# Kernel tuning notes

Measured on AMD Instinct MI355X. Metric: run time of the kernel, lower is better.

The kernel has to match this reference:

```python
import jax, jax.numpy as jnp
import numpy as np

B, N, ADA, L, D_OUT, C_T, N_DIS = 8, 2048, 16, 64, 16, 4, 8
H = L // D_OUT  # 4 heads emulated via split/cat on the batch dim


def setup_inputs() -> dict:
    key = jax.random.key(0)
    ks = jax.random.split(key, 12)
    f = lambda i, shape, s=1.0: jax.random.normal(ks[i], shape, dtype=jnp.float32) * s
    return dict(
        c=f(0, (B, N, L)),
        c_condition=f(1, (B, C_T)),
        c_disease=f(2, (B, N_DIS)),
        state=f(3, (B, N, L)),
        emb_normal=f(4, (N, ADA)),                 # nn.Parameter embeddings_normal
        W_q1=f(5, (C_T, L), 0.1), b_q1=jnp.zeros((L,), jnp.float32),
        W_qr1=f(6, (1, L), 0.1),  b_qr1=jnp.zeros((L,), jnp.float32),
        W_q2=f(7, (L, L), 0.1),   b_q2=jnp.zeros((L,), jnp.float32),
        W_qr2=f(8, (L, L), 0.1),  b_qr2=jnp.zeros((L,), jnp.float32),
        Wp_gcn=f(9, (ADA, 2, L, L), 0.1),          # adaptive weight pool (cheb_k=2)
        bp_gcn=f(10, (ADA, L), 0.1),               # adaptive bias pool
    )


def _to_heads(t):
    # torch.cat(torch.split(t, D_OUT, dim=-1), dim=0): [B,N,H*d] -> [H*B,N,d]
    return jnp.concatenate(jnp.split(t, H, axis=-1), axis=0)


def _from_heads(t):
    # inverse: [H*B,N,d] -> [B,N,H*d]
    return jnp.concatenate(jnp.split(t, H, axis=0), axis=-1)


def _anode_gcn(x, E, Wp, bp):
    # adaptive GCN (AGCRN-style AVWGCN): supports=[I, softmax(relu(E E^T))]
    A = jax.nn.softmax(jax.nn.relu(E @ E.T), axis=1)          # [N,N]
    xg = jnp.stack([x, jnp.einsum('nm,bmc->bnc', A, x)], 1)   # [B,2,N,C]
    Wn = jnp.einsum('nd,dkio->nkio', E, Wp)                   # per-node weights
    bn = E @ bp                                               # [N,L]
    return jnp.einsum('bkni,nkio->bno', xg, Wn) + bn


def reference(c, c_condition, c_disease, state, emb_normal,
              W_q1, b_q1, W_qr1, b_qr1, W_q2, b_q2, W_qr2, b_qr2,
              Wp_gcn, bp_gcn):
    # gated query path
    Qt = jax.nn.sigmoid(c_condition[:, None, :] @ W_q1 + b_q1)        # [B,1,L]
    Qt = jnp.tanh((Qt * c) @ W_q2 + b_q2)                             # [B,N,L]
    # disease loop vectorized: sum_n sigmoid(Linear(c_disease[:, n:n+1]))
    qr = jax.nn.sigmoid(c_disease[:, :, None] * W_qr1[0] + b_qr1)     # [B,D,L]
    qr = qr.sum(axis=1, keepdims=True)                                # [B,1,L]
    qr = Qt + jnp.tanh((qr * c) @ W_qr2 + b_qr2)                      # [B,N,L]
    qr_h = _to_heads(qr)  # computed in the original but unused in output

    theta = _to_heads(state)                                          # [HB,N,d]
    ct = jnp.tanh(_anode_gcn(c, emb_normal, Wp_gcn, bp_gcn))          # [B,N,L]
    ct = _to_heads(ct)                                                # [HB,N,d]

    attn = jnp.einsum('bnd,bmd->bnm', theta, theta) / jnp.sqrt(jnp.float32(D_OUT))
    attn = jax.nn.softmax(attn, axis=-1)                              # [HB,N,N]
    x = -jnp.einsum('bnm,bmd->bnd', attn, ct)                         # [HB,N,d]
    return _from_heads(x)                                             # [B,N,L]
```

## Files before the change

### kernel.cpp

```cpp
#include <hip/hip_runtime.h>
#include <hip/hip_bf16.h>

#define NN 2048
#define BB 8
#define LL 64
#define ADA 16
#define DH 16
#define HB 32
#define KT 2048
#define CGSZ ((size_t)BB * NN * LL)

typedef __attribute__((ext_vector_type(4))) short bf16x4;
typedef __attribute__((ext_vector_type(4))) float f32x4;
typedef _Float16 half_t;
typedef __attribute__((ext_vector_type(2))) _Float16 halfx2;
typedef __attribute__((ext_vector_type(4))) _Float16 halfx4;
typedef __attribute__((ext_vector_type(8))) _Float16 halfx8;

#if defined(__HIP_DEVICE_COMPILE__)
#if __has_builtin(__builtin_amdgcn_mfma_f32_16x16x16f16)
#define MFMA16H(a, b, c) __builtin_amdgcn_mfma_f32_16x16x16f16(a, b, c, 0, 0, 0)
#elif __has_builtin(__builtin_amdgcn_mfma_f32_16x16x16_f16)
#define MFMA16H(a, b, c) __builtin_amdgcn_mfma_f32_16x16x16_f16(a, b, c, 0, 0, 0)
#else
#error "no 16x16x16 f16 mfma builtin on device"
#endif
#if __has_builtin(__builtin_amdgcn_mfma_f32_16x16x32_f16)
#define MFMA32H(a, b, c) __builtin_amdgcn_mfma_f32_16x16x32_f16(a, b, c, 0, 0, 0)
#else
#error "no 16x16x32 f16 mfma builtin on device"
#endif
#if __has_builtin(__builtin_amdgcn_exp2f)
#define EXP2F(x) __builtin_amdgcn_exp2f(x)
#else
#define EXP2F(x) exp2f(x)
#endif
#else
#define MFMA16H(a, b, c) (c)
#define MFMA32H(a, b, c) (c)
#define EXP2F(x) exp2f(x)
#endif

__device__ inline halfx2 cvt_pk2(float a, float b) {
#if defined(__HIP_DEVICE_COMPILE__) && __has_builtin(__builtin_amdgcn_cvt_pkrtz)
  auto r = __builtin_amdgcn_cvt_pkrtz(a, b);
  return __builtin_bit_cast(halfx2, r);
#else
  halfx2 r;
  r[0] = (_Float16)a;
  r[1] = (_Float16)b;
  return r;
#endif
}

__device__ inline float tanh_fast(float v) {
  return 1.f - 2.f / (__expf(2.f * v) + 1.f);
}

__global__ __launch_bounds__(256) void k_preps(const float* __restrict__ E,
                                               const float* __restrict__ c,
                                               const float* __restrict__ state,
                                               const float* __restrict__ Wp,
                                               half_t* __restrict__ A16,
                                               half_t* __restrict__ cT16,
                                               half_t* __restrict__ WpT,
                                               half_t* __restrict__ th16h,
                                               half_t* __restrict__ thq16h) {
  __shared__ float sbuf[4 * 2304];
  const int id = blockIdx.x;
  const int t = threadIdx.x;
  if (id < 512) {
    float(*row)[NN] = (float(*)[NN])sbuf;
    float(*red)[256] = (float(*)[256])(sbuf + 4 * NN);
    const int n = id * 4;
    float4 e[4][4];
#pragma unroll
    for (int r = 0; r < 4; ++r) {
      const float4* Er = (const float4*)(E + (size_t)(n + r) * ADA);
#pragma unroll
      for (int j = 0; j < 4; ++j) e[r][j] = Er[j];
    }
    float l[4] = {0.f, 0.f, 0.f, 0.f};
    for (int m = t; m < NN; m += 256) {
      const float4* Em = (const float4*)(E + (size_t)m * ADA);
      float4 ev[4];
#pragma unroll
      for (int j = 0; j < 4; ++j) ev[j] = Em[j];
#pragma unroll
      for (int r = 0; r < 4; ++r) {
        float s = 0.f;
#pragma unroll
        for (int j = 0; j < 4; ++j) {
          s = fmaf(e[r][j].x, ev[j].x, s);
          s = fmaf(e[r][j].y, ev[j].y, s);
          s = fmaf(e[r][j].z, ev[j].z, s);
          s = fmaf(e[r][j].w, ev[j].w, s);
        }
        float p = __expf(fmaxf(s, 0.f) - 20.f);
        row[r][m] = p;
        l[r] += p;
      }
    }
#pragma unroll
    for (int r = 0; r < 4; ++r) red[r][t] = l[r];
    __syncthreads();
    for (int off = 128; off > 0; off >>= 1) {
      if (t < off) {
#pragma unroll
        for (int r = 0; r < 4; ++r) red[r][t] += red[r][t + off];
      }
      __syncthreads();
    }
    float inv[4];
#pragma unroll
    for (int r = 0; r < 4; ++r) inv[r] = 1.f / red[r][0];
    for (int m = t; m < NN; m += 256) {
#pragma unroll
      for (int r = 0; r < 4; ++r)
        A16[(size_t)(n + r) * NN + m] = (half_t)(row[r][m] * inv[r]);
    }
  } else if (id < 768) {
    float(*ld)[68] = (float(*)[68])sbuf;
    const int idx = id - 512;
    const int m0 = (idx & 31) * 64;
    const int b = idx >> 5;
    {
      const int r = t & 63, cq = t >> 6;
      const float* cp = c + ((size_t)b * NN + m0 + r) * LL + cq * 16;
#pragma unroll
      for (int u = 0; u < 4; ++u)
        *(float4*)&ld[r][cq * 16 + 4 * u] = *(const float4*)(cp + 4 * u);
    }
    __syncthreads();
    const int o = t & 63, mq = t >> 6;
    halfx8 h0, h1;
#pragma unroll
    for (int v = 0; v < 8; ++v) {
      h0[v] = (half_t)ld[mq * 16 + v][o];
      h1[v] = (half_t)ld[mq * 16 + 8 + v][o];
    }
    half_t* op = cT16 + ((size_t)b * LL + o) * NN + m0 + mq * 16;
    *(halfx8*)op = h0;
    *(halfx8*)(op + 8) = h1;
  } else if (id < 800) {
    float(*ld)[68] = (float(*)[68])sbuf;
    const int k0 = (id - 768) * 64;
    {
      const int r = t & 63, cq = t >> 6;
      const float* wp = Wp + (size_t)(k0 + r) * LL + cq * 16;
#pragma unroll
      for (int u = 0; u < 4; ++u)
        *(float4*)&ld[r][cq * 16 + 4 * u] = *(const float4*)(wp + 4 * u);
    }
    __syncthreads();
    const int o = t & 63, kq = t >> 6;
    halfx8 h0, h1;
#pragma unroll
    for (int v = 0; v < 8; ++v) {
      h0[v] = (half_t)ld[kq * 16 + v][o];
      h1[v] = (half_t)ld[kq * 16 + 8 + v][o];
    }
    half_t* op = WpT + (size_t)o * KT + k0 + kq * 16;
    *(halfx8*)op = h0;
    *(halfx8*)(op + 8) = h1;
  } else {
    const int idx = id - 800;
    const int n0 = (idx & 31) * 64;
    const int b = idx >> 5;
    const int r = t >> 2, h = t & 3;
    const float QS = 0.25f * 1.4426950408889634f;
    const float* sp = state + ((size_t)b * NN + n0 + r) * LL + h * DH;
    half_t tk[16], tq[16];
#pragma unroll
    for (int u = 0; u < 4; ++u) {
      float4 sv = *(const float4*)(sp + 4 * u);
      tk[4 * u + 0] = (half_t)sv.x; tk[4 * u + 1] = (half_t)sv.y;
      tk[4 * u + 2] = (half_t)sv.z; tk[4 * u + 3] = (half_t)sv.w;
      tq[4 * u + 0] = (half_t)(QS * sv.x); tq[4 * u + 1] = (half_t)(QS * sv.y);
      tq[4 * u + 2] = (half_t)(QS * sv.z); tq[4 * u + 3] = (half_t)(QS * sv.w);
    }
    const size_t base = ((size_t)(h * 8 + b) * NN + n0 + r) * DH;
    *(halfx8*)(th16h + base) = *(const halfx8*)&tk[0];
    *(halfx8*)(th16h + base + 8) = *(const halfx8*)&tk[8];
    *(halfx8*)(thq16h + base) = *(const halfx8*)&tq[0];
    *(halfx8*)(thq16h + base + 8) = *(const halfx8*)&tq[8];
  }
}

__global__ __launch_bounds__(256) void k_gemm1b(const half_t* __restrict__ A16,
                                                const half_t* __restrict__ cT16,
                                                float* __restrict__ cg) {
  __shared__ half_t sA[64][72];
  __shared__ half_t sB[2][64][72];
  const int t = threadIdx.x;
  const int n0 = blockIdx.x * 64;
  const int b0 = blockIdx.y * 2;
  const int kh = blockIdx.z;
  const int wv = t >> 6, lane = t & 63;
  const int lr = lane & 15, lg = lane >> 4;
  const half_t* cb0 = cT16 + (size_t)b0 * LL * NN;
  const half_t* cb1 = cb0 + (size_t)LL * NN;
  const int sr = t >> 2, sc = (t & 3) * 16;
  f32x4 acc[2][4];
#pragma unroll
  for (int bb = 0; bb < 2; ++bb)
#pragma unroll
    for (int ot = 0; ot < 4; ++ot) acc[bb][ot] = (f32x4){0.f, 0.f, 0.f, 0.f};

  for (int k0 = kh * (NN / 4); k0 < (kh + 1) * (NN / 4); k0 += 64) {
    __syncthreads();
    {
      const half_t* ga = A16 + (size_t)(n0 + sr) * NN + k0 + sc;
      *(halfx8*)&sA[sr][sc] = *(const halfx8*)ga;
      *(halfx8*)&sA[sr][sc + 8] = *(const halfx8*)(ga + 8);
      const half_t* g0 = cb0 + (size_t)sr * NN + k0 + sc;
      *(halfx8*)&sB[0][sr][sc] = *(const halfx8*)g0;
      *(halfx8*)&sB[0][sr][sc + 8] = *(const halfx8*)(g0 + 8);
      const half_t* g1 = cb1 + (size_t)sr * NN + k0 + sc;
      *(halfx8*)&sB[1][sr][sc] = *(const halfx8*)g1;
      *(halfx8*)&sB[1][sr][sc + 8] = *(const halfx8*)(g1 + 8);
    }
    __syncthreads();
#pragma unroll
    for (int kt = 0; kt < 2; ++kt) {
      halfx8 a = *(const halfx8*)&sA[16 * wv + lr][kt * 32 + 8 * lg];
#pragma unroll
      for (int bb = 0; bb < 2; ++bb) {
#pragma unroll
        for (int ot = 0; ot < 4; ++ot) {
          halfx8 bq = *(const halfx8*)&sB[bb][ot * 16 + lr][kt * 32 + 8 * lg];
          acc[bb][ot] = MFMA32H(a, bq, acc[bb][ot]);
        }
      }
    }
  }
#pragma unroll
  for (int bb = 0; bb < 2; ++bb) {
    float* outp = cg + (size_t)kh * CGSZ + ((size_t)(b0 + bb) * NN + n0 + 16 * wv) * LL;
#pragma unroll
    for (int ot = 0; ot < 4; ++ot)
#pragma unroll
      for (int reg = 0; reg < 4; ++reg)
        outp[(size_t)(4 * lg + reg) * LL + ot * 16 + lr] = acc[bb][ot][reg];
  }
}

__global__ __launch_bounds__(256) void k_gcn4(const float* __restrict__ E,
                                              const half_t* __restrict__ WpT,
                                              const float* __restrict__ bp,
                                              const float* __restrict__ c,
                                              const float* __restrict__ cg,
                                              half_t* __restrict__ vt16h) {
  __shared__ half_t sW[32][136];
  __shared__ float sE[64][17];
  __shared__ float sbp[16][32];
  const int t = threadIdx.x;
  const int n0 = blockIdx.x * 64;
  const int b = blockIdx.y;
  const int oh = blockIdx.z;
  const int wv = t >> 6, lane = t & 63;
  const int lr = lane & 15, lg = lane >> 4;
  {
    const int r = t >> 2, dq = (t & 3) * 4;
    float4 ev = *(const float4*)(E + (size_t)(n0 + r) * ADA + dq);
    sE[r][dq + 0] = ev.x; sE[r][dq + 1] = ev.y;
    sE[r][dq + 2] = ev.z; sE[r][dq + 3] = ev.w;
    const int d = t >> 4, o2 = (t & 15) * 2;
    float2 bv = *(const float2*)(bp + d * LL + oh * 32 + o2);
    sbp[d][o2] = bv.x;
    sbp[d][o2 + 1] = bv.y;
  }
  float xr[4][8];
  {
    const size_t rbase = ((size_t)b * NN + n0 + 16 * wv + lr) * LL;
#pragma unroll
    for (int u = 0; u < 2; ++u) {
      const float* p = c + rbase + u * 32 + 8 * lg;
      float4 v0 = *(const float4*)p, v1 = *(const float4*)(p + 4);
      xr[u][0] = v0.x; xr[u][1] = v0.y; xr[u][2] = v0.z; xr[u][3] = v0.w;
      xr[u][4] = v1.x; xr[u][5] = v1.y; xr[u][6] = v1.z; xr[u][7] = v1.w;
    }
#pragma unroll
    for (int u = 0; u < 2; ++u) {
      const size_t off = rbase + u * 32 + 8 * lg;
      float4 a0 = *(const float4*)(cg + off), a1 = *(const float4*)(cg + off + 4);
      float4 b0 = *(const float4*)(cg + CGSZ + off), b1 = *(const float4*)(cg + CGSZ + off + 4);
      float4 c0 = *(const float4*)(cg + 2 * CGSZ + off), c1 = *(const float4*)(cg + 2 * CGSZ + off + 4);
      float4 d0 = *(const float4*)(cg + 3 * CGSZ + off), d1 = *(const float4*)(cg + 3 * CGSZ + off + 4);
      xr[2 + u][0] = (a0.x + b0.x) + (c0.x + d0.x);
      xr[2 + u][1] = (a0.y + b0.y) + (c0.y + d0.y);
      xr[2 + u][2] = (a0.z + b0.z) + (c0.z + d0.z);
      xr[2 + u][3] = (a0.w + b0.w) + (c0.w + d0.w);
      xr[2 + u][4] = (a1.x + b1.x) + (c1.x + d1.x);
      xr[2 + u][5] = (a1.y + b1.y) + (c1.y + d1.y);
      xr[2 + u][6] = (a1.z + b1.z) + (c1.z + d1.z);
      xr[2 + u][7] = (a1.w + b1.w) + (c1.w + d1.w);
    }
  }
  __syncthreads();
  f32x4 acc[2];
#pragma unroll
  for (int ot2 = 0; ot2 < 2; ++ot2) {
    f32x4 s = (f32x4){0.f, 0.f, 0.f, 0.f};
#pragma unroll
    for (int d = 0; d < ADA; ++d) {
      const float bpv = sbp[d][ot2 * 16 + lr];
#pragma unroll
      for (int reg = 0; reg < 4; ++reg)
        s[reg] = fmaf(sE[16 * wv + 4 * lg + reg][d], bpv, s[reg]);
    }
    acc[ot2] = s;
  }
  const int so = t >> 3, sq = t & 7;
  halfx8 wreg[2];
  {
    const half_t* p = WpT + (size_t)(oh * 32 + so) * KT + sq * 16;
    wreg[0] = *(const halfx8*)p;
    wreg[1] = *(const halfx8*)(p + 8);
  }
  for (int dd = 0; dd < ADA; ++dd) {
    __syncthreads();
    *(halfx8*)&sW[so][sq * 16] = wreg[0];
    *(halfx8*)&sW[so][sq * 16 + 8] = wreg[1];
    __syncthreads();
    if (dd < ADA - 1) {
      const half_t* p = WpT + (size_t)(oh * 32 + so) * KT + (dd + 1) * 128 + sq * 16;
      wreg[0] = *(const halfx8*)p;
      wreg[1] = *(const halfx8*)(p + 8);
    }
    const float e = sE[16 * wv + lr][dd];
    halfx8 af[4];
#pragma unroll
    for (int kt = 0; kt < 4; ++kt)
#pragma unroll
      for (int j = 0; j < 8; ++j) af[kt][j] = (half_t)(e * xr[kt][j]);
#pragma unroll
    for (int kt = 0; kt < 4; ++kt) {
#pragma unroll
      for (int ot2 = 0; ot2 < 2; ++ot2) {
        halfx8 bq = *(const halfx8*)&sW[ot2 * 16 + lr][kt * 32 + 8 * lg];
        acc[ot2] = MFMA32H(af[kt], bq, acc[ot2]);
      }
    }
  }
#pragma unroll
  for (int ot2 = 0; ot2 < 2; ++ot2) {
    const int h = oh * 2 + ot2;
    halfx4 o4;
#pragma unroll
    for (int reg = 0; reg < 4; ++reg) o4[reg] = (half_t)tanh_fast(acc[ot2][reg]);
    *(halfx4*)(vt16h + ((size_t)(h * 8 + b) * DH + lr) * NN + n0 + 16 * wv + 4 * lg) = o4;
  }
}

__global__ __launch_bounds__(512, 4) void k_attn5(const half_t* __restrict__ th16h,
                                                  const half_t* __restrict__ thq16h,
                                                  const half_t* __restrict__ vt16h,
                                                  float* __restrict__ out) {
  __shared__ float sred[8][8][16][16];
  float* dfl = &sred[0][0][0][0];
  const int hb = blockIdx.x;
  const int h = hb >> 3, b = hb & 7;
  const int wv = threadIdx.x >> 6, lane = threadIdx.x & 63;
  const int q0 = blockIdx.y * 128;
  const int lr = lane & 15, lg = lane >> 4;
  const half_t* th = th16h + (size_t)hb * NN * DH;
  const half_t* thq = thq16h + (size_t)hb * NN * DH;
  const half_t* vrow = vt16h + ((size_t)hb * DH + lr) * NN;
  halfx4 qf[8];
#pragma unroll
  for (int f = 0; f < 8; ++f)
    qf[f] = *(const halfx4*)(thq + (size_t)(q0 + 16 * f + lr) * DH + 4 * lg);
  const float SH = 8.f * 1.4426950408889634f;
  const f32x4 shiftv = {-SH, -SH, -SH, -SH};
  f32x4 acc[8];
  float den[8];
#pragma unroll
  for (int f = 0; f < 8; ++f) { acc[f] = (f32x4){0.f, 0.f, 0.f, 0.f}; den[f] = 0.f; }

  const int mb = wv * (NN / 8);
  halfx4 kf = *(const halfx4*)(th + (size_t)(mb + lr) * DH + 4 * lg);
  halfx4 vf = *(const halfx4*)(vrow + mb + 4 * lg);
  for (int mt = 0; mt < NN / 128; ++mt) {
    halfx4 kf_n = kf, vf_n = vf;
    if (mt < NN / 128 - 1) {
      const int mn = mb + (mt + 1) * 16;
      kf_n = *(const halfx4*)(th + (size_t)(mn + lr) * DH + 4 * lg);
      vf_n = *(const halfx4*)(vrow + mn + 4 * lg);
    }
#pragma unroll
    for (int f = 0; f < 8; ++f) {
      f32x4 s = MFMA16H(kf, qf[f], shiftv);
      float p0 = EXP2F(s[0]), p1 = EXP2F(s[1]), p2 = EXP2F(s[2]), p3 = EXP2F(s[3]);
      den[f] += (p0 + p1) + (p2 + p3);
      halfx2 lo = cvt_pk2(p0, p1), hi = cvt_pk2(p2, p3);
      halfx4 pf;
      pf[0] = lo[0]; pf[1] = lo[1]; pf[2] = hi[0]; pf[3] = hi[1];
      acc[f] = MFMA16H(pf, vf, acc[f]);
    }
    kf = kf_n; vf = vf_n;
  }
#pragma unroll
  for (int f = 0; f < 8; ++f) {
    den[f] += __shfl_xor(den[f], 16);
    den[f] += __shfl_xor(den[f], 32);
  }
  if (lane < 16) {
#pragma unroll
    for (int f = 0; f < 8; ++f) dfl[(wv * 8 + f) * 16 + lane] = den[f];
  }
  __syncthreads();
  const int t = threadIdx.x;
  const int fo = t >> 6, ro = (t >> 2) & 15, duo = (t & 3) * 4;
  float ds = 0.f;
#pragma unroll
  for (int w = 0; w < 8; ++w) ds += dfl[(w * 8 + fo) * 16 + ro];
  __syncthreads();
#pragma unroll
  for (int f = 0; f < 8; ++f) {
#pragma unroll
    for (int reg = 0; reg < 4; ++reg) sred[wv][f][4 * lg + reg][lr] = acc[f][reg];
  }
  __syncthreads();
  float4 ns = make_float4(0.f, 0.f, 0.f, 0.f);
#pragma unroll
  for (int w = 0; w < 8; ++w) {
    float4 v = *(const float4*)&sred[w][fo][ro][duo];
    ns.x += v.x; ns.y += v.y; ns.z += v.z; ns.w += v.w;
  }
  const float inv = -1.f / ds;
  float4 o = make_float4(ns.x * inv, ns.y * inv, ns.z * inv, ns.w * inv);
  *(float4*)(out + ((size_t)b * NN + q0 + 16 * fo + ro) * LL + h * DH + duo) = o;
}

extern "C" void kernel_launch(void* const* d_in, const int* in_sizes, int n_in,
                              void* d_out, int out_size, void* d_ws, size_t ws_size,
                              hipStream_t stream) {
  const float* c = (const float*)d_in[0];
  const float* state = (const float*)d_in[3];
  const float* E = (const float*)d_in[4];
  const float* Wp = (const float*)d_in[13];
  const float* bp = (const float*)d_in[14];
  float* out = (float*)d_out;

  half_t* A16 = (half_t*)d_ws;
  half_t* cT16 = A16 + (size_t)NN * NN;
  half_t* WpT = cT16 + (size_t)BB * LL * NN;
  float* cg = (float*)(WpT + (size_t)LL * KT);
  half_t* th16h = (half_t*)(cg + 4 * CGSZ);
  half_t* thq16h = th16h + (size_t)HB * NN * DH;
  half_t* vt16h = thq16h + (size_t)HB * NN * DH;

  k_preps<<<1056, 256, 0, stream>>>(E, c, state, Wp, A16, cT16, WpT, th16h, thq16h);
  k_gemm1b<<<dim3(NN / 64, BB / 2, 4), 256, 0, stream>>>(A16, cT16, cg);
  k_gcn4<<<dim3(NN / 64, BB, 2), 256, 0, stream>>>(E, WpT, bp, c, cg, vt16h);
  k_attn5<<<dim3(HB, NN / 128), 512, 0, stream>>>(th16h, thq16h, vt16h, out);
}
```

Before: 67.87 us.

## Split attention key range across two blocks with separate reduction kernel

The attention kernel now splits the key dimension into two halves via a third grid dimension. Each block writes partial numerators and denominators to workspace, and a new reduction kernel combines them, normalizes, and writes the output. This doubles the block count from 512 to 1024 so the GPU is better occupied. The cost is an extra launch plus partial-sum traffic through global memory. The fixed exp shift keeps the split-softmax combination exact.

```diff
diff --git a/kernel.cpp b/kernel.cpp
--- a/kernel.cpp
+++ b/kernel.cpp
@@ -353,16 +353,17 @@
   }
 }
 
-__global__ __launch_bounds__(512, 4) void k_attn5(const half_t* __restrict__ th16h,
+__global__ __launch_bounds__(512, 4) void k_attn6(const half_t* __restrict__ th16h,
                                                   const half_t* __restrict__ thq16h,
                                                   const half_t* __restrict__ vt16h,
-                                                  float* __restrict__ out) {
+                                                  float* __restrict__ npart,
+                                                  float* __restrict__ dpart) {
   __shared__ float sred[8][8][16][16];
   float* dfl = &sred[0][0][0][0];
   const int hb = blockIdx.x;
-  const int h = hb >> 3, b = hb & 7;
   const int wv = threadIdx.x >> 6, lane = threadIdx.x & 63;
   const int q0 = blockIdx.y * 128;
+  const int mz = blockIdx.z;
   const int lr = lane & 15, lg = lane >> 4;
   const half_t* th = th16h + (size_t)hb * NN * DH;
   const half_t* thq = thq16h + (size_t)hb * NN * DH;
@@ -378,12 +379,12 @@
 #pragma unroll
   for (int f = 0; f < 8; ++f) { acc[f] = (f32x4){0.f, 0.f, 0.f, 0.f}; den[f] = 0.f; }
 
-  const int mb = wv * (NN / 8);
+  const int mb = mz * (NN / 2) + wv * (NN / 16);
   halfx4 kf = *(const halfx4*)(th + (size_t)(mb + lr) * DH + 4 * lg);
   halfx4 vf = *(const halfx4*)(vrow + mb + 4 * lg);
-  for (int mt = 0; mt < NN / 128; ++mt) {
+  for (int mt = 0; mt < NN / 256; ++mt) {
     halfx4 kf_n = kf, vf_n = vf;
-    if (mt < NN / 128 - 1) {
+    if (mt < NN / 256 - 1) {
       const int mn = mb + (mt + 1) * 16;
       kf_n = *(const halfx4*)(th + (size_t)(mn + lr) * DH + 4 * lg);
       vf_n = *(const halfx4*)(vrow + mn + 4 * lg);
@@ -428,9 +429,28 @@
     float4 v = *(const float4*)&sred[w][fo][ro][duo];
     ns.x += v.x; ns.y += v.y; ns.z += v.z; ns.w += v.w;
   }
+  const int q = q0 + 16 * fo + ro;
+  *(float4*)(npart + (((size_t)mz * HB + hb) * NN + q) * DH + duo) = ns;
+  if (duo == 0) dpart[((size_t)mz * HB + hb) * NN + q] = ds;
+}
+
+__global__ __launch_bounds__(256) void k_red(const float* __restrict__ npart,
+                                             const float* __restrict__ dpart,
+                                             float* __restrict__ out) {
+  const int idx = blockIdx.x * 256 + threadIdx.x;
+  const int row = idx >> 2;
+  const int du = (idx & 3) * 4;
+  const int hb = row >> 11, q = row & 2047;
+  const int h = hb >> 3, b = hb & 7;
+  const size_t base0 = ((size_t)row) * DH + du;
+  const size_t base1 = ((size_t)HB * NN + row) * DH + du;
+  float4 n0 = *(const float4*)(npart + base0);
+  float4 n1 = *(const float4*)(npart + base1);
+  const float ds = dpart[row] + dpart[(size_t)HB * NN + row];
   const float inv = -1.f / ds;
-  float4 o = make_float4(ns.x * inv, ns.y * inv, ns.z * inv, ns.w * inv);
-  *(float4*)(out + ((size_t)b * NN + q0 + 16 * fo + ro) * LL + h * DH + duo) = o;
+  float4 o = make_float4((n0.x + n1.x) * inv, (n0.y + n1.y) * inv,
+                         (n0.z + n1.z) * inv, (n0.w + n1.w) * inv);
+  *(float4*)(out + ((size_t)b * NN + q) * LL + h * DH + du) = o;
 }
 
 extern "C" void kernel_launch(void* const* d_in, const int* in_sizes, int n_in,
@@ -450,9 +470,12 @@
   half_t* th16h = (half_t*)(cg + 4 * CGSZ);
   half_t* thq16h = th16h + (size_t)HB * NN * DH;
   half_t* vt16h = thq16h + (size_t)HB * NN * DH;
+  float* npart = (float*)(vt16h + (size_t)HB * NN * DH);
+  float* dpart = npart + (size_t)2 * HB * NN * DH;
 
   k_preps<<<1056, 256, 0, stream>>>(E, c, state, Wp, A16, cT16, WpT, th16h, thq16h);
   k_gemm1b<<<dim3(NN / 64, BB / 2, 4), 256, 0, stream>>>(A16, cT16, cg);
   k_gcn4<<<dim3(NN / 64, BB, 2), 256, 0, stream>>>(E, WpT, bp, c, cg, vt16h);
-  k_attn5<<<dim3(HB, NN / 128), 512, 0, stream>>>(th16h, thq16h, vt16h, out);
-}
+  k_attn6<<<dim3(HB, NN / 128, 2), 512, 0, stream>>>(th16h, thq16h, vt16h, npart, dpart);
+  k_red<<<(HB * NN * 4) / 256, 256, 0, stream>>>(npart, dpart, out);
+}
```

Result: slower. 71.45 us (+5.3%).
